# Performance work log

Hardware: AMD Instinct MI355X
Metric: run time of the kernel (lower is better)

Reference implementation:

```python
import jax, jax.numpy as jnp
import numpy as np

SIGMA = 1.0

def setup_inputs() -> dict:
    key = jax.random.key(0)
    k1, k2 = jax.random.split(key)
    N, IN, OUT = 524288, 64, 128
    x = jax.random.normal(k1, (N, IN), dtype=jnp.float32)
    bin_centers = jax.random.normal(k2, (OUT, IN), dtype=jnp.float32)
    return {"x": x, "bin_centers": bin_centers}

def reference(x, bin_centers):
    # distances[n,o] = sum_i (x[n,i] - c[o,i])^2 = ||x_n||^2 - 2 x_n.c_o + ||c_o||^2
    x2 = jnp.sum(x * x, axis=1)[:, None]                # [N,1]
    c2 = jnp.sum(bin_centers * bin_centers, axis=1)[None, :]  # [1,O]
    xc = jnp.einsum('ni,oi->no', x, bin_centers)        # [N,O] GEMM
    distances = x2 - 2.0 * xc + c2                      # [N,O]
    rbf = jnp.exp(-distances / (2.0 * SIGMA ** 2))      # [N,O]
    # histogram[o,i] = sum_n rbf[n,o] * x[n,i]  ->  rbf^T @ x
    histogram = jnp.einsum('no,ni->oi', rbf, x)         # [O,I] GEMM
    return histogram
```

## Files before the change

kernel.cpp:

```cpp
#include <hip/hip_runtime.h>
#include <stdint.h>


typedef _Float16 half8v __attribute__((ext_vector_type(8)));
typedef _Float16 half4v __attribute__((ext_vector_type(4)));
typedef __fp16  fp16x2 __attribute__((ext_vector_type(2)));
typedef float floatx4 __attribute__((ext_vector_type(4)));

#define GRIDN 512
#define NITER 32
#define LOG2E 1.4426950408889634f
#define PBIAS 38.0f
#define PUNSCALE 3.637978807091713e-12f

#if __has_builtin(__builtin_amdgcn_exp2f)
#define EXP2F(x) __builtin_amdgcn_exp2f(x)
#else
#define EXP2F(x) exp2f(x)
#endif

static __device__ __forceinline__ unsigned int pk16z(float a, float b) {
  fp16x2 h = __builtin_amdgcn_cvt_pkrtz(a, b);
  return __builtin_bit_cast(unsigned int, h);
}
static __device__ __forceinline__ unsigned int pk16(float a, float b) {
  unsigned short ha = __builtin_bit_cast(unsigned short, (_Float16)a);
  unsigned short hb = __builtin_bit_cast(unsigned short, (_Float16)b);
  return (unsigned int)ha | ((unsigned int)hb << 16);
}
static __device__ __forceinline__ half4v mkh4(unsigned int lo, unsigned int hi) {
  uint2 u{lo, hi};
  return __builtin_bit_cast(half4v, u);
}
static __device__ __forceinline__ half8v mkh8(unsigned int a, unsigned int b,
                                              unsigned int c, unsigned int d) {
  uint4 u{a, b, c, d};
  return __builtin_bit_cast(half8v, u);
}

static __device__ __forceinline__ floatx4 mfma32(half8v a, half8v b, floatx4 c) {
  return __builtin_amdgcn_mfma_f32_16x16x32_f16(a, b, c, 0, 0, 0);
}
static __device__ __forceinline__ floatx4 mfma16(half4v a, half4v b, floatx4 c) {
  return __builtin_amdgcn_mfma_f32_16x16x16f16(a, b, c, 0, 0, 0);
}

#define LSTR 72

__global__ __launch_bounds__(256, 4) void rbf_hist_kernel(
    const float* __restrict__ x, const float* __restrict__ c,
    float* __restrict__ out) {
  __shared__ unsigned short sXh[2][32][LSTR];
  __shared__ float          sX2[2][32];

  const int t    = threadIdx.x;
  const int lane = t & 63;
  const int w    = t >> 6;
  const int l15  = lane & 15;
  const int quad = lane >> 4;

  half8v chi[2][2];
  float m2c[2];
#pragma unroll
  for (int oo = 0; oo < 2; ++oo) {
    const int ot = 2 * w + oo;
    float sq = 0.f;
#pragma unroll
    for (int s = 0; s < 2; ++s) {
      const float* p = c + (ot * 16 + l15) * 64 + s * 32 + quad * 8;
      float4 va = *(const float4*)(p);
      float4 vb = *(const float4*)(p + 4);
      float f[8] = {va.x, va.y, va.z, va.w, vb.x, vb.y, vb.z, vb.w};
      unsigned int h[4];
#pragma unroll
      for (int jp = 0; jp < 4; ++jp) {
        float a = f[2 * jp], b = f[2 * jp + 1];
        sq = fmaf(a, a, sq);
        sq = fmaf(b, b, sq);
        h[jp] = pk16(a * LOG2E, b * LOG2E);
      }
      chi[oo][s] = mkh8(h[0], h[1], h[2], h[3]);
    }
    sq += __shfl_xor(sq, 16);
    sq += __shfl_xor(sq, 32);
    m2c[oo] = fmaf(-0.5f * LOG2E, sq, PBIAS);
  }

  half4v iden;
  {
    float e0 = (quad * 4 + 0 == l15) ? 1.f : 0.f;
    float e1 = (quad * 4 + 1 == l15) ? 1.f : 0.f;
    float e2 = (quad * 4 + 2 == l15) ? 1.f : 0.f;
    float e3 = (quad * 4 + 3 == l15) ? 1.f : 0.f;
    iden = mkh4(pk16z(e0, e1), pk16z(e2, e3));
  }

  floatx4 hacc[2][4];
#pragma unroll
  for (int a = 0; a < 2; ++a)
#pragma unroll
    for (int b = 0; b < 4; ++b) {
      floatx4 z = {0.f, 0.f, 0.f, 0.f};
      hacc[a][b] = z;
    }

  const int r = t >> 3, q = t & 7;

  auto stage = [&](int B, float4 v0, float4 v1) {
    float f0 = v0.x, f1 = v0.y, f2 = v0.z, f3 = v0.w;
    float f4 = v1.x, f5 = v1.y, f6 = v1.z, f7 = v1.w;
    float sq = 0.f;
    sq = fmaf(f0, f0, sq); sq = fmaf(f1, f1, sq);
    sq = fmaf(f2, f2, sq); sq = fmaf(f3, f3, sq);
    sq = fmaf(f4, f4, sq); sq = fmaf(f5, f5, sq);
    sq = fmaf(f6, f6, sq); sq = fmaf(f7, f7, sq);
    *(uint4*)&sXh[B][r][q * 8] =
        uint4{pk16(f0, f1), pk16(f2, f3), pk16(f4, f5), pk16(f6, f7)};
    sq += __shfl_xor(sq, 1);
    sq += __shfl_xor(sq, 2);
    sq += __shfl_xor(sq, 4);
    if (q == 0) sX2[B][r] = -0.5f * LOG2E * sq;
  };

  auto compute = [&](int B) {
#pragma unroll
    for (int t2 = 0; t2 < 2; ++t2) {
      half8v xh0 = *(const half8v*)&sXh[B][t2 * 16 + l15][quad * 8];
      half8v xh1 = *(const half8v*)&sXh[B][t2 * 16 + l15][32 + quad * 8];
      float4 m2x = *(const float4*)&sX2[B][t2 * 16 + quad * 4];

      half4v P[2];
#pragma unroll
      for (int oo = 0; oo < 2; ++oo) {
        floatx4 acc = {m2x.x + m2c[oo], m2x.y + m2c[oo],
                       m2x.z + m2c[oo], m2x.w + m2c[oo]};
        acc = mfma32(xh0, chi[oo][0], acc);
        acc = mfma32(xh1, chi[oo][1], acc);
        P[oo] = mkh4(pk16z(EXP2F(acc[0]), EXP2F(acc[1])),
                     pk16z(EXP2F(acc[2]), EXP2F(acc[3])));
      }

      half4v XT[4];
#pragma unroll
      for (int itl = 0; itl < 4; ++itl) {
        half4v ax = *(const half4v*)&sXh[B][t2 * 16 + l15][itl * 16 + quad * 4];
        floatx4 z = {0.f, 0.f, 0.f, 0.f};
        floatx4 d = mfma16(ax, iden, z);
        XT[itl] = mkh4(pk16z(d[0], d[1]), pk16z(d[2], d[3]));
      }

#pragma unroll
      for (int oo = 0; oo < 2; ++oo)
#pragma unroll
        for (int itl = 0; itl < 4; ++itl)
          hacc[oo][itl] = mfma16(P[oo], XT[itl], hacc[oo][itl]);
    }
  };

  {
    const float* p0 = x + ((size_t)blockIdx.x * 32 + r) * 64 + q * 8;
    float4 a0 = *(const float4*)(p0);
    float4 a1 = *(const float4*)(p0 + 4);
    const float* p1 =
        x + ((size_t)(blockIdx.x + GRIDN) * 32 + r) * 64 + q * 8;
    float4 b0 = *(const float4*)(p1);
    float4 b1 = *(const float4*)(p1 + 4);
    stage(0, a0, a1);
    stage(1, b0, b1);
  }
  float4 rA[2], rB[2];
  {
    const float* pA =
        x + ((size_t)(blockIdx.x + 2 * GRIDN) * 32 + r) * 64 + q * 8;
    rA[0] = *(const float4*)(pA);
    rA[1] = *(const float4*)(pA + 4);
    const float* pB =
        x + ((size_t)(blockIdx.x + 3 * GRIDN) * 32 + r) * 64 + q * 8;
    rB[0] = *(const float4*)(pB);
    rB[1] = *(const float4*)(pB + 4);
  }
  __syncthreads();

#pragma unroll 1
  for (int it = 0; it < NITER; it += 2) {
    compute(0);
    __syncthreads();
    if (it + 2 < NITER) stage(0, rA[0], rA[1]);
    if (it + 4 < NITER) {
      const float* p = x +
          ((size_t)(blockIdx.x + (size_t)(it + 4) * GRIDN) * 32 + r) * 64 +
          q * 8;
      rA[0] = *(const float4*)(p);
      rA[1] = *(const float4*)(p + 4);
    }
    compute(1);
    __syncthreads();
    if (it + 3 < NITER) stage(1, rB[0], rB[1]);
    if (it + 5 < NITER) {
      const float* p = x +
          ((size_t)(blockIdx.x + (size_t)(it + 5) * GRIDN) * 32 + r) * 64 +
          q * 8;
      rB[0] = *(const float4*)(p);
      rB[1] = *(const float4*)(p + 4);
    }
  }

#pragma unroll
  for (int oo = 0; oo < 2; ++oo)
#pragma unroll
    for (int itl = 0; itl < 4; ++itl)
#pragma unroll
      for (int e = 0; e < 4; ++e) {
        int o = (2 * w + oo) * 16 + quad * 4 + e;
        int i = itl * 16 + l15;
        atomicAdd(out + o * 64 + i, hacc[oo][itl][e] * PUNSCALE);
      }
}

__global__ void zero_out_kernel(float* out, int n) {
  int i = blockIdx.x * 256 + threadIdx.x;
  if (i < n) out[i] = 0.f;
}

extern "C" void kernel_launch(void* const* d_in, const int* in_sizes, int n_in,
                              void* d_out, int out_size, void* d_ws, size_t ws_size,
                              hipStream_t stream) {
  (void)in_sizes; (void)n_in; (void)d_ws; (void)ws_size;
  const float* x = (const float*)d_in[0];
  const float* c = (const float*)d_in[1];
  float* out = (float*)d_out;

  zero_out_kernel<<<(out_size + 255) / 256, 256, 0, stream>>>(out, out_size);
  rbf_hist_kernel<<<GRIDN, 256, 0, stream>>>(x, c, out);
}
```

Before: 199.8 us.

## Split waves by row half and four output tiles, merge partial histograms in LDS

Each wave now handles one 16-row half of the 32-row tile across four output tiles, where before it handled both row halves across two output tiles. This halves the shared-memory X reads per output tile and doubles the histogram accumulators per wave, so launch bounds drop to 2 blocks per SM. At the end, paired waves merge their partial histograms through a 32KB LDS buffer before atomically adding to global memory, which halves the global atomics. The cost is higher register pressure, lower occupancy, and an extra LDS merge step.

After: 202.4 us. Within noise of the previous version (+1.3%).

```diff
diff --git a/kernel.cpp b/kernel.cpp
--- a/kernel.cpp
+++ b/kernel.cpp
@@ -47,23 +47,26 @@
 
 #define LSTR 72
 
-__global__ __launch_bounds__(256, 4) void rbf_hist_kernel(
+__global__ __launch_bounds__(256, 2) void rbf_hist_kernel(
     const float* __restrict__ x, const float* __restrict__ c,
     float* __restrict__ out) {
   __shared__ unsigned short sXh[2][32][LSTR];
   __shared__ float          sX2[2][32];
+  __shared__ float          sMerge[2][4096];
 
   const int t    = threadIdx.x;
   const int lane = t & 63;
   const int w    = t >> 6;
   const int l15  = lane & 15;
   const int quad = lane >> 4;
-
-  half8v chi[2][2];
-  float m2c[2];
-#pragma unroll
-  for (int oo = 0; oo < 2; ++oo) {
-    const int ot = 2 * w + oo;
+  const int t2c  = w & 1;
+  const int ob   = (w >> 1) * 4;
+
+  half8v chi[4][2];
+  float m2c[4];
+#pragma unroll
+  for (int oo = 0; oo < 4; ++oo) {
+    const int ot = ob + oo;
     float sq = 0.f;
 #pragma unroll
     for (int s = 0; s < 2; ++s) {
@@ -95,9 +98,9 @@
     iden = mkh4(pk16z(e0, e1), pk16z(e2, e3));
   }
 
-  floatx4 hacc[2][4];
-#pragma unroll
-  for (int a = 0; a < 2; ++a)
+  floatx4 hacc[4][4];
+#pragma unroll
+  for (int a = 0; a < 4; ++a)
 #pragma unroll
     for (int b = 0; b < 4; ++b) {
       floatx4 z = {0.f, 0.f, 0.f, 0.f};
@@ -123,38 +126,35 @@
   };
 
   auto compute = [&](int B) {
-#pragma unroll
-    for (int t2 = 0; t2 < 2; ++t2) {
-      half8v xh0 = *(const half8v*)&sXh[B][t2 * 16 + l15][quad * 8];
-      half8v xh1 = *(const half8v*)&sXh[B][t2 * 16 + l15][32 + quad * 8];
-      float4 m2x = *(const float4*)&sX2[B][t2 * 16 + quad * 4];
-
-      half4v P[2];
-#pragma unroll
-      for (int oo = 0; oo < 2; ++oo) {
-        floatx4 acc = {m2x.x + m2c[oo], m2x.y + m2c[oo],
-                       m2x.z + m2c[oo], m2x.w + m2c[oo]};
-        acc = mfma32(xh0, chi[oo][0], acc);
-        acc = mfma32(xh1, chi[oo][1], acc);
-        P[oo] = mkh4(pk16z(EXP2F(acc[0]), EXP2F(acc[1])),
-                     pk16z(EXP2F(acc[2]), EXP2F(acc[3])));
-      }
-
-      half4v XT[4];
-#pragma unroll
-      for (int itl = 0; itl < 4; ++itl) {
-        half4v ax = *(const half4v*)&sXh[B][t2 * 16 + l15][itl * 16 + quad * 4];
-        floatx4 z = {0.f, 0.f, 0.f, 0.f};
-        floatx4 d = mfma16(ax, iden, z);
-        XT[itl] = mkh4(pk16z(d[0], d[1]), pk16z(d[2], d[3]));
-      }
-
-#pragma unroll
-      for (int oo = 0; oo < 2; ++oo)
-#pragma unroll
-        for (int itl = 0; itl < 4; ++itl)
-          hacc[oo][itl] = mfma16(P[oo], XT[itl], hacc[oo][itl]);
-    }
+    half8v xh0 = *(const half8v*)&sXh[B][t2c * 16 + l15][quad * 8];
+    half8v xh1 = *(const half8v*)&sXh[B][t2c * 16 + l15][32 + quad * 8];
+    float4 m2x = *(const float4*)&sX2[B][t2c * 16 + quad * 4];
+
+    half4v P[4];
+#pragma unroll
+    for (int oo = 0; oo < 4; ++oo) {
+      floatx4 acc = {m2x.x + m2c[oo], m2x.y + m2c[oo],
+                     m2x.z + m2c[oo], m2x.w + m2c[oo]};
+      acc = mfma32(xh0, chi[oo][0], acc);
+      acc = mfma32(xh1, chi[oo][1], acc);
+      P[oo] = mkh4(pk16z(EXP2F(acc[0]), EXP2F(acc[1])),
+                   pk16z(EXP2F(acc[2]), EXP2F(acc[3])));
+    }
+
+    half4v XT[4];
+#pragma unroll
+    for (int itl = 0; itl < 4; ++itl) {
+      half4v ax = *(const half4v*)&sXh[B][t2c * 16 + l15][itl * 16 + quad * 4];
+      floatx4 z = {0.f, 0.f, 0.f, 0.f};
+      floatx4 d = mfma16(ax, iden, z);
+      XT[itl] = mkh4(pk16z(d[0], d[1]), pk16z(d[2], d[3]));
+    }
+
+#pragma unroll
+    for (int oo = 0; oo < 4; ++oo)
+#pragma unroll
+      for (int itl = 0; itl < 4; ++itl)
+        hacc[oo][itl] = mfma16(P[oo], XT[itl], hacc[oo][itl]);
   };
 
   {
@@ -205,16 +205,33 @@
     }
   }
 
-#pragma unroll
-  for (int oo = 0; oo < 2; ++oo)
-#pragma unroll
-    for (int itl = 0; itl < 4; ++itl)
-#pragma unroll
-      for (int e = 0; e < 4; ++e) {
-        int o = (2 * w + oo) * 16 + quad * 4 + e;
-        int i = itl * 16 + l15;
-        atomicAdd(out + o * 64 + i, hacc[oo][itl][e] * PUNSCALE);
-      }
+  const int pair = w >> 1;
+  __syncthreads();
+  if (w & 1) {
+#pragma unroll
+    for (int oo = 0; oo < 4; ++oo)
+#pragma unroll
+      for (int itl = 0; itl < 4; ++itl)
+#pragma unroll
+        for (int e = 0; e < 4; ++e)
+          sMerge[pair][((oo * 4 + itl) * 16 + quad * 4 + e) * 16 + l15] =
+              hacc[oo][itl][e];
+  }
+  __syncthreads();
+  if (!(w & 1)) {
+#pragma unroll
+    for (int oo = 0; oo < 4; ++oo)
+#pragma unroll
+      for (int itl = 0; itl < 4; ++itl)
+#pragma unroll
+        for (int e = 0; e < 4; ++e) {
+          int o = (ob + oo) * 16 + quad * 4 + e;
+          int i = itl * 16 + l15;
+          float v = hacc[oo][itl][e] +
+                    sMerge[pair][((oo * 4 + itl) * 16 + quad * 4 + e) * 16 + l15];
+          atomicAdd(out + o * 64 + i, v * PUNSCALE);
+        }
+  }
 }
 
 __global__ void zero_out_kernel(float* out, int n) {
```

## Use 128-thread blocks with 4 output tiles per wave and double grid

Applied to the files above, without the earlier changes.

Each block now runs 2 waves instead of 4, and each wave owns 4 output-column tiles instead of 2. This halves the number of waves that recompute the X transpose and the LDS reads per row tile. The grid doubles to 1024 blocks with half the iterations each, so total work is unchanged but atomics at the end double. Register pressure rises from the larger accumulator and centre arrays, and the launch-bounds occupancy hint changes.

After: 215.6 us. 1.08x slower.

```diff
diff --git a/kernel.cpp b/kernel.cpp
--- a/kernel.cpp
+++ b/kernel.cpp
@@ -7,8 +7,8 @@
 typedef __fp16  fp16x2 __attribute__((ext_vector_type(2)));
 typedef float floatx4 __attribute__((ext_vector_type(4)));
 
-#define GRIDN 512
-#define NITER 32
+#define GRIDN 1024
+#define NITER 16
 #define LOG2E 1.4426950408889634f
 #define PBIAS 38.0f
 #define PUNSCALE 3.637978807091713e-12f
@@ -47,7 +47,7 @@
 
 #define LSTR 72
 
-__global__ __launch_bounds__(256, 4) void rbf_hist_kernel(
+__global__ __launch_bounds__(128, 2) void rbf_hist_kernel(
     const float* __restrict__ x, const float* __restrict__ c,
     float* __restrict__ out) {
   __shared__ unsigned short sXh[2][32][LSTR];
@@ -58,12 +58,13 @@
   const int w    = t >> 6;
   const int l15  = lane & 15;
   const int quad = lane >> 4;
-
-  half8v chi[2][2];
-  float m2c[2];
-#pragma unroll
-  for (int oo = 0; oo < 2; ++oo) {
-    const int ot = 2 * w + oo;
+  const int ob   = w * 4;
+
+  half8v chi[4][2];
+  float m2c[4];
+#pragma unroll
+  for (int oo = 0; oo < 4; ++oo) {
+    const int ot = ob + oo;
     float sq = 0.f;
 #pragma unroll
     for (int s = 0; s < 2; ++s) {
@@ -95,30 +96,37 @@
     iden = mkh4(pk16z(e0, e1), pk16z(e2, e3));
   }
 
-  floatx4 hacc[2][4];
-#pragma unroll
-  for (int a = 0; a < 2; ++a)
+  floatx4 hacc[4][4];
+#pragma unroll
+  for (int a = 0; a < 4; ++a)
 #pragma unroll
     for (int b = 0; b < 4; ++b) {
       floatx4 z = {0.f, 0.f, 0.f, 0.f};
       hacc[a][b] = z;
     }
 
-  const int r = t >> 3, q = t & 7;
-
-  auto stage = [&](int B, float4 v0, float4 v1) {
-    float f0 = v0.x, f1 = v0.y, f2 = v0.z, f3 = v0.w;
-    float f4 = v1.x, f5 = v1.y, f6 = v1.z, f7 = v1.w;
+  const int r = t >> 2, q = t & 3;
+
+  auto stage = [&](int B, const float4* v) {
+    float f0 = v[0].x, f1 = v[0].y, f2 = v[0].z, f3 = v[0].w;
+    float f4 = v[1].x, f5 = v[1].y, f6 = v[1].z, f7 = v[1].w;
+    float f8 = v[2].x, f9 = v[2].y, fa = v[2].z, fb = v[2].w;
+    float fc = v[3].x, fd = v[3].y, fe = v[3].z, ff = v[3].w;
     float sq = 0.f;
     sq = fmaf(f0, f0, sq); sq = fmaf(f1, f1, sq);
     sq = fmaf(f2, f2, sq); sq = fmaf(f3, f3, sq);
     sq = fmaf(f4, f4, sq); sq = fmaf(f5, f5, sq);
     sq = fmaf(f6, f6, sq); sq = fmaf(f7, f7, sq);
-    *(uint4*)&sXh[B][r][q * 8] =
+    sq = fmaf(f8, f8, sq); sq = fmaf(f9, f9, sq);
+    sq = fmaf(fa, fa, sq); sq = fmaf(fb, fb, sq);
+    sq = fmaf(fc, fc, sq); sq = fmaf(fd, fd, sq);
+    sq = fmaf(fe, fe, sq); sq = fmaf(ff, ff, sq);
+    *(uint4*)&sXh[B][r][q * 16] =
         uint4{pk16(f0, f1), pk16(f2, f3), pk16(f4, f5), pk16(f6, f7)};
+    *(uint4*)&sXh[B][r][q * 16 + 8] =
+        uint4{pk16(f8, f9), pk16(fa, fb), pk16(fc, fd), pk16(fe, ff)};
     sq += __shfl_xor(sq, 1);
     sq += __shfl_xor(sq, 2);
-    sq += __shfl_xor(sq, 4);
     if (q == 0) sX2[B][r] = -0.5f * LOG2E * sq;
   };
 
@@ -129,9 +137,9 @@
       half8v xh1 = *(const half8v*)&sXh[B][t2 * 16 + l15][32 + quad * 8];
       float4 m2x = *(const float4*)&sX2[B][t2 * 16 + quad * 4];
 
-      half4v P[2];
-#pragma unroll
-      for (int oo = 0; oo < 2; ++oo) {
+      half4v P[4];
+#pragma unroll
+      for (int oo = 0; oo < 4; ++oo) {
         floatx4 acc = {m2x.x + m2c[oo], m2x.y + m2c[oo],
                        m2x.z + m2c[oo], m2x.w + m2c[oo]};
         acc = mfma32(xh0, chi[oo][0], acc);
@@ -150,7 +158,7 @@
       }
 
 #pragma unroll
-      for (int oo = 0; oo < 2; ++oo)
+      for (int oo = 0; oo < 4; ++oo)
 #pragma unroll
         for (int itl = 0; itl < 4; ++itl)
           hacc[oo][itl] = mfma16(P[oo], XT[itl], hacc[oo][itl]);
@@ -158,26 +166,35 @@
   };
 
   {
-    const float* p0 = x + ((size_t)blockIdx.x * 32 + r) * 64 + q * 8;
-    float4 a0 = *(const float4*)(p0);
-    float4 a1 = *(const float4*)(p0 + 4);
+    float4 a[4], b[4];
+    const float* p0 = x + ((size_t)blockIdx.x * 32 + r) * 64 + q * 16;
+    a[0] = *(const float4*)(p0);
+    a[1] = *(const float4*)(p0 + 4);
+    a[2] = *(const float4*)(p0 + 8);
+    a[3] = *(const float4*)(p0 + 12);
     const float* p1 =
-        x + ((size_t)(blockIdx.x + GRIDN) * 32 + r) * 64 + q * 8;
-    float4 b0 = *(const float4*)(p1);
-    float4 b1 = *(const float4*)(p1 + 4);
-    stage(0, a0, a1);
-    stage(1, b0, b1);
-  }
-  float4 rA[2], rB[2];
+        x + ((size_t)(blockIdx.x + GRIDN) * 32 + r) * 64 + q * 16;
+    b[0] = *(const float4*)(p1);
+    b[1] = *(const float4*)(p1 + 4);
+    b[2] = *(const float4*)(p1 + 8);
+    b[3] = *(const float4*)(p1 + 12);
+    stage(0, a);
+    stage(1, b);
+  }
+  float4 rA[4], rB[4];
   {
     const float* pA =
-        x + ((size_t)(blockIdx.x + 2 * GRIDN) * 32 + r) * 64 + q * 8;
+        x + ((size_t)(blockIdx.x + 2 * GRIDN) * 32 + r) * 64 + q * 16;
     rA[0] = *(const float4*)(pA);
     rA[1] = *(const float4*)(pA + 4);
+    rA[2] = *(const float4*)(pA + 8);
+    rA[3] = *(const float4*)(pA + 12);
     const float* pB =
-        x + ((size_t)(blockIdx.x + 3 * GRIDN) * 32 + r) * 64 + q * 8;
+        x + ((size_t)(blockIdx.x + 3 * GRIDN) * 32 + r) * 64 + q * 16;
     rB[0] = *(const float4*)(pB);
     rB[1] = *(const float4*)(pB + 4);
+    rB[2] = *(const float4*)(pB + 8);
+    rB[3] = *(const float4*)(pB + 12);
   }
   __syncthreads();
 
@@ -185,33 +202,37 @@
   for (int it = 0; it < NITER; it += 2) {
     compute(0);
     __syncthreads();
-    if (it + 2 < NITER) stage(0, rA[0], rA[1]);
+    if (it + 2 < NITER) stage(0, rA);
     if (it + 4 < NITER) {
       const float* p = x +
           ((size_t)(blockIdx.x + (size_t)(it + 4) * GRIDN) * 32 + r) * 64 +
-          q * 8;
+          q * 16;
       rA[0] = *(const float4*)(p);
       rA[1] = *(const float4*)(p + 4);
+      rA[2] = *(const float4*)(p + 8);
+      rA[3] = *(const float4*)(p + 12);
     }
     compute(1);
     __syncthreads();
-    if (it + 3 < NITER) stage(1, rB[0], rB[1]);
+    if (it + 3 < NITER) stage(1, rB);
     if (it + 5 < NITER) {
       const float* p = x +
           ((size_t)(blockIdx.x + (size_t)(it + 5) * GRIDN) * 32 + r) * 64 +
-          q * 8;
+          q * 16;
       rB[0] = *(const float4*)(p);
       rB[1] = *(const float4*)(p + 4);
-    }
-  }
-
-#pragma unroll
-  for (int oo = 0; oo < 2; ++oo)
+      rB[2] = *(const float4*)(p + 8);
+      rB[3] = *(const float4*)(p + 12);
+    }
+  }
+
+#pragma unroll
+  for (int oo = 0; oo < 4; ++oo)
 #pragma unroll
     for (int itl = 0; itl < 4; ++itl)
 #pragma unroll
       for (int e = 0; e < 4; ++e) {
-        int o = (2 * w + oo) * 16 + quad * 4 + e;
+        int o = (ob + oo) * 16 + quad * 4 + e;
         int i = itl * 16 + l15;
         atomicAdd(out + o * 64 + i, hacc[oo][itl][e] * PUNSCALE);
       }
@@ -231,5 +252,5 @@
   float* out = (float*)d_out;
 
   zero_out_kernel<<<(out_size + 255) / 256, 256, 0, stream>>>(out, out_size);
-  rbf_hist_kernel<<<GRIDN, 256, 0, stream>>>(x, c, out);
-}
+  rbf_hist_kernel<<<GRIDN, 128, 0, stream>>>(x, c, out);
+}
```
